# Kernel optimization log

Hardware: AMD Instinct MI355X
Metric: run time of the kernel (lower is better)

Reference implementation:

```python
import jax, jax.numpy as jnp
import numpy as np

N = 33_554_432
NUM_CLASSES = 10


def setup_inputs() -> dict:
    key = jax.random.key(0)
    k1, k2, k3 = jax.random.split(key, 3)
    predictions = jax.random.normal(k1, (N,), dtype=jnp.float32)
    labels = jax.random.randint(k2, (N,), 0, NUM_CLASSES, dtype=jnp.int32)
    weights = jax.random.uniform(k3, (NUM_CLASSES,), dtype=jnp.float32)
    return {"predictions": predictions, "labels": labels, "weights": weights}


def reference(predictions, labels, weights):
    # per-element weighted squared error: weights[label] * (pred - label)^2, then mean
    diff = predictions - labels.astype(predictions.dtype)
    w = weights[labels]  # gather per-class weight
    return jnp.mean(w * diff * diff)
```

## Files before the change

kernel.cpp:

```cpp
#include <hip/hip_runtime.h>

#define NBLOCKS 2048
#define NTHREADS 256
#define ITERS 16

typedef float fvec4 __attribute__((ext_vector_type(4)));
typedef int   ivec4 __attribute__((ext_vector_type(4)));
typedef double dvec2 __attribute__((ext_vector_type(2)));

__device__ __forceinline__ fvec4 ntloadf(const fvec4* p) {
    return __builtin_nontemporal_load(p);
}
__device__ __forceinline__ ivec4 ntloadi(const ivec4* p) {
    return __builtin_nontemporal_load(p);
}

__global__ __launch_bounds__(NTHREADS) void wmse_kernel(
    const fvec4* __restrict__ pred4,
    const ivec4* __restrict__ lab4,
    const float* __restrict__ weights,
    double* __restrict__ partials,
    int n4)
{
    __shared__ float w[16];
    if (threadIdx.x < 10) w[threadIdx.x] = weights[threadIdx.x];
    __syncthreads();

    const int S = NBLOCKS * NTHREADS;
    const int t = blockIdx.x * NTHREADS + threadIdx.x;

    double acc = 0.0;

    if (n4 == S * ITERS) {
        #pragma unroll 4
        for (int k = 0; k < ITERS; ++k) {
            const int idx = t + k * S;
            fvec4 p = ntloadf(pred4 + idx);
            ivec4 l = ntloadi(lab4 + idx);
            float d0 = p.x - (float)l.x, d1 = p.y - (float)l.y;
            float d2 = p.z - (float)l.z, d3 = p.w - (float)l.w;
            float s = w[l.x]*d0*d0 + w[l.y]*d1*d1
                    + w[l.z]*d2*d2 + w[l.w]*d3*d3;
            acc += (double)s;
        }
    } else {
        for (int i = t; i < n4; i += S) {
            fvec4 p = pred4[i];
            ivec4 l = lab4[i];
            float d0 = p.x - (float)l.x, d1 = p.y - (float)l.y;
            float d2 = p.z - (float)l.z, d3 = p.w - (float)l.w;
            acc += (double)(w[l.x]*d0*d0 + w[l.y]*d1*d1
                          + w[l.z]*d2*d2 + w[l.w]*d3*d3);
        }
    }

    for (int off = 32; off > 0; off >>= 1)
        acc += __shfl_down(acc, off, 64);

    __shared__ double wave_sums[NTHREADS / 64];
    int lane = threadIdx.x & 63;
    int wid  = threadIdx.x >> 6;
    if (lane == 0) wave_sums[wid] = acc;
    __syncthreads();

    if (threadIdx.x == 0) {
        double tsum = 0.0;
        #pragma unroll
        for (int k = 0; k < NTHREADS / 64; ++k) tsum += wave_sums[k];
        partials[blockIdx.x] = tsum;
    }
}

#define FTHREADS 1024

__global__ __launch_bounds__(FTHREADS) void wmse_final_kernel(
    const dvec2* __restrict__ partials2,
    float* __restrict__ out,
    double inv_n)
{
    double acc = 0.0;
    #pragma unroll
    for (int k = 0; k < NBLOCKS / 2 / FTHREADS; ++k) {
        dvec2 v = partials2[threadIdx.x + k * FTHREADS];
        acc += v.x + v.y;
    }

    for (int off = 32; off > 0; off >>= 1)
        acc += __shfl_down(acc, off, 64);

    __shared__ double wave_sums[FTHREADS / 64];
    int lane = threadIdx.x & 63;
    int wid  = threadIdx.x >> 6;
    if (lane == 0) wave_sums[wid] = acc;
    __syncthreads();

    if (threadIdx.x == 0) {
        double t = 0.0;
        #pragma unroll
        for (int k = 0; k < FTHREADS / 64; ++k) t += wave_sums[k];
        out[0] = (float)(t * inv_n);
    }
}

extern "C" void kernel_launch(void* const* d_in, const int* in_sizes, int n_in,
                              void* d_out, int out_size, void* d_ws, size_t ws_size,
                              hipStream_t stream) {
    const float* pred    = (const float*)d_in[0];
    const int*   labels  = (const int*)d_in[1];
    const float* weights = (const float*)d_in[2];
    float* out = (float*)d_out;

    int n  = in_sizes[0];
    int n4 = n >> 2;

    double* partials = (double*)d_ws;

    wmse_kernel<<<NBLOCKS, NTHREADS, 0, stream>>>(
        (const fvec4*)pred, (const ivec4*)labels, weights, partials, n4);

    wmse_final_kernel<<<1, FTHREADS, 0, stream>>>(
        (const dvec2*)partials, out, 1.0 / (double)n);
}
```

Measured before the change: 254.4 us.

## Stage loads through LDS with async global_load_lds double buffering

Replaces the direct nontemporal vector loads with asynchronous global-to-LDS copies (global_load_lds, 16 bytes per lane) into a per-wave double buffer. The next chunk is prefetched while the current one is read back from LDS and reduced, using explicit vmcnt waits. This aims to keep more memory requests in flight for a bandwidth-bound reduction, at the cost of extra LDS traffic and reliance on per-wave ordering of vmcnt and LDS writes without a barrier.

```diff
diff --git a/kernel.cpp b/kernel.cpp
--- a/kernel.cpp
+++ b/kernel.cpp
@@ -2,17 +2,18 @@
 
 #define NBLOCKS 2048
 #define NTHREADS 256
-#define ITERS 16
+#define WAVES (NTHREADS / 64)
+#define CHUNKS 16
 
 typedef float fvec4 __attribute__((ext_vector_type(4)));
 typedef int   ivec4 __attribute__((ext_vector_type(4)));
 typedef double dvec2 __attribute__((ext_vector_type(2)));
 
-__device__ __forceinline__ fvec4 ntloadf(const fvec4* p) {
-    return __builtin_nontemporal_load(p);
-}
-__device__ __forceinline__ ivec4 ntloadi(const ivec4* p) {
-    return __builtin_nontemporal_load(p);
+typedef const __attribute__((address_space(1))) unsigned int guint;
+typedef __attribute__((address_space(3))) unsigned int luint;
+
+__device__ __forceinline__ void stage16(const void* gptr, void* ldsptr) {
+    __builtin_amdgcn_global_load_lds((guint*)gptr, (luint*)ldsptr, 16, 0, 2 );
 }
 
 __global__ __launch_bounds__(NTHREADS) void wmse_kernel(
@@ -23,20 +24,37 @@
     int n4)
 {
     __shared__ float w[16];
+    __shared__ fvec4 lds_p[2][WAVES][64];
+    __shared__ ivec4 lds_l[2][WAVES][64];
+
     if (threadIdx.x < 10) w[threadIdx.x] = weights[threadIdx.x];
     __syncthreads();
 
+    const int lane = threadIdx.x & 63;
+    const int wid  = threadIdx.x >> 6;
     const int S = NBLOCKS * NTHREADS;
     const int t = blockIdx.x * NTHREADS + threadIdx.x;
 
     double acc = 0.0;
 
-    if (n4 == S * ITERS) {
-        #pragma unroll 4
-        for (int k = 0; k < ITERS; ++k) {
-            const int idx = t + k * S;
-            fvec4 p = ntloadf(pred4 + idx);
-            ivec4 l = ntloadi(lab4 + idx);
+    if (n4 == S * CHUNKS) {
+        stage16(pred4 + t, &lds_p[0][wid][0]);
+        stage16(lab4  + t, &lds_l[0][wid][0]);
+
+        #pragma unroll
+        for (int k = 0; k < CHUNKS; ++k) {
+            const int cur = k & 1;
+            if (k + 1 < CHUNKS) {
+                const int nxt = (k + 1) & 1;
+                const int idx = t + (k + 1) * S;
+                stage16(pred4 + idx, &lds_p[nxt][wid][0]);
+                stage16(lab4  + idx, &lds_l[nxt][wid][0]);
+                asm volatile("s_waitcnt vmcnt(2)" ::: "memory");
+            } else {
+                asm volatile("s_waitcnt vmcnt(0)" ::: "memory");
+            }
+            fvec4 p = lds_p[cur][wid][lane];
+            ivec4 l = lds_l[cur][wid][lane];
             float d0 = p.x - (float)l.x, d1 = p.y - (float)l.y;
             float d2 = p.z - (float)l.z, d3 = p.w - (float)l.w;
             float s = w[l.x]*d0*d0 + w[l.y]*d1*d1
@@ -57,16 +75,14 @@
     for (int off = 32; off > 0; off >>= 1)
         acc += __shfl_down(acc, off, 64);
 
-    __shared__ double wave_sums[NTHREADS / 64];
-    int lane = threadIdx.x & 63;
-    int wid  = threadIdx.x >> 6;
+    __shared__ double wave_sums[WAVES];
     if (lane == 0) wave_sums[wid] = acc;
     __syncthreads();
 
     if (threadIdx.x == 0) {
         double tsum = 0.0;
         #pragma unroll
-        for (int k = 0; k < NTHREADS / 64; ++k) tsum += wave_sums[k];
+        for (int k = 0; k < WAVES; ++k) tsum += wave_sums[k];
         partials[blockIdx.x] = tsum;
     }
 }
```

Result: no change. 252.9 us (-0.6%).
